# Kernel optimization log

Measured on AMD Instinct MI355X. Metric: run time of the kernel, lower is better.

## Reference

```python
import jax, jax.numpy as jnp
import numpy as np

D = 768  # hidden dim hard-coded in the module


def setup_inputs() -> dict:
    key = jax.random.key(0)
    k1, k2, k3, k4, k5 = jax.random.split(key, 5)
    N, M = 512, 512
    return {
        "text_output": jax.random.normal(k1, (N, D), dtype=jnp.float32),
        "visual_output": jax.random.normal(k2, (M, D), dtype=jnp.float32),
        "W1": jax.random.normal(k3, (D, D), dtype=jnp.float32),
        "W2": jax.random.normal(k4, (D, D), dtype=jnp.float32),
        "W3": jax.random.normal(k5, (D, D), dtype=jnp.float32),
    }


def reference(text_output, visual_output, W1, W2, W3):
    # C[n,m] = tanh( (text @ W1) . visual[m] )
    C = jnp.tanh((text_output @ W1) @ visual_output.T)            # (N, M)
    W2_text = text_output @ W2                                    # (N, D)
    W3_visual = visual_output @ W3.T                              # (M, D)
    # M[n,m,:] = tanh(W2_text[n] + W3_visual[m] * C[n,m])
    Mt = jnp.tanh(W2_text[:, None, :] + W3_visual[None, :, :] * C[..., None])  # (N, M, D)
    # score[n,m] = text[n] . M[n,m]  (replaces the per-row Python loop)
    score = jnp.einsum("nd,nmd->nm", text_output, Mt)             # (N, M)
    return score
```

## Files before the change

### kernel.cpp

```cpp
#include <hip/hip_runtime.h>

#define DD   768
#define NN   512
#define MM   512

#define PRE_K 2.88539008177792681472f

typedef _Float16 h8 __attribute__((ext_vector_type(8)));
typedef __attribute__((ext_vector_type(4))) float f32x4;

__device__ __forceinline__ float fexp(float x) { return __builtin_amdgcn_exp2f(x); }
__device__ __forceinline__ float frcp(float x) { return __builtin_amdgcn_rcpf(x); }
__device__ __forceinline__ float fast_tanh(float x) {
  return 1.0f - 2.0f * frcp(fexp(PRE_K * x) + 1.0f);
}

__device__ __forceinline__ void splitf(float x, ushort& h, ushort& l) {
  const _Float16 hh = (_Float16)x;
  const _Float16 ll = (_Float16)(x - (float)hh);
  h = __builtin_bit_cast(unsigned short, hh);
  l = __builtin_bit_cast(unsigned short, ll);
}

__global__ __launch_bounds__(256) void prep_kernel(
    const float* __restrict__ text, const float* __restrict__ visual,
    const float* __restrict__ W1, const float* __restrict__ W2,
    const float* __restrict__ W3,
    ushort* __restrict__ th, ushort* __restrict__ tl,
    ushort* __restrict__ vh, ushort* __restrict__ vl,
    ushort* __restrict__ w3h, ushort* __restrict__ w3l,
    ushort* __restrict__ w1th, ushort* __restrict__ w1tl,
    ushort* __restrict__ w2th, ushort* __restrict__ w2tl,
    float* __restrict__ out)
{
  __shared__ float Lt[32][33];
  const int b = blockIdx.x;
  const int t = threadIdx.x;

  if (b < 1344) {
    const float* src; ushort *dh, *dl; size_t off;
    if (b < 384)      { src = text;   dh = th;  dl = tl;  off = (size_t)b * 1024; }
    else if (b < 768) { src = visual; dh = vh;  dl = vl;  off = (size_t)(b - 384) * 1024; }
    else              { src = W3;     dh = w3h; dl = w3l; off = (size_t)(b - 768) * 1024; }
    const size_t i = off + (size_t)t * 4;
    const float4 v = *(const float4*)&src[i];
    ushort4 h, l;
    splitf(v.x, h.x, l.x); splitf(v.y, h.y, l.y);
    splitf(v.z, h.z, l.z); splitf(v.w, h.w, l.w);
    *(ushort4*)&dh[i] = h;
    *(ushort4*)&dl[i] = l;
  } else if (b < 2496) {
    const int tt = b - 1344;
    const bool second = tt >= 576;
    const int tile = second ? tt - 576 : tt;
    const float* W = second ? W2 : W1;
    ushort* oh = second ? w2th : w1th;
    ushort* ol = second ? w2tl : w1tl;
    const int k0 = (tile / 24) * 32, j0 = (tile % 24) * 32;
    {
      const int k = t >> 3, j4 = (t & 7) * 4;
      const float4 v = *(const float4*)&W[(size_t)(k0 + k) * DD + j0 + j4];
      Lt[j4 + 0][k] = v.x; Lt[j4 + 1][k] = v.y;
      Lt[j4 + 2][k] = v.z; Lt[j4 + 3][k] = v.w;
    }
    __syncthreads();
    {
      const int j = t >> 3, k4 = (t & 7) * 4;
      ushort4 h, l;
      splitf(Lt[j][k4 + 0], h.x, l.x); splitf(Lt[j][k4 + 1], h.y, l.y);
      splitf(Lt[j][k4 + 2], h.z, l.z); splitf(Lt[j][k4 + 3], h.w, l.w);
      *(ushort4*)&oh[(size_t)(j0 + j) * DD + k0 + k4] = h;
      *(ushort4*)&ol[(size_t)(j0 + j) * DD + k0 + k4] = l;
    }
  } else {
    float* red = (float*)Lt;
    const int u = b - 2496;
    const int n0 = u * 2;
    const int half = t >> 7;
    const int lt = t & 127;

    const float* tr = text + (size_t)(n0 + half) * DD;
    float s = 0.f;
    #pragma unroll
    for (int i = 0; i < DD / 128; ++i) s += tr[lt + i * 128];
    red[t] = s;
    __syncthreads();
    #pragma unroll
    for (int st = 64; st > 0; st >>= 1) {
      if (lt < st) red[t] += red[t + st];
      __syncthreads();
    }
    const float Tn = red[half << 7];
    float4 o; o.x = Tn; o.y = Tn; o.z = Tn; o.w = Tn;
    *(float4*)&out[(size_t)(n0 + half) * MM + lt * 4] = o;
  }
}

#define BK   32
#define LROW 40
#define APL  (32 * LROW)
#define BPL  (64 * LROW)

template <bool ALO>
__device__ __forceinline__ void gemm_core32(
    ushort* __restrict__ As, ushort* __restrict__ Bs,
    const ushort* __restrict__ Ahg, const ushort* __restrict__ Alg,
    const ushort* __restrict__ Bhg, const ushort* __restrict__ Blg,
    int i0, int j0, int nsteps, f32x4* acc)
{
  const int tid = threadIdx.x;
  const int row = tid >> 2;
  const int ks8 = (tid & 3) * 8;
  const bool doA = (row < 32);
  const size_t ga = (size_t)(i0 + row) * DD + ks8;
  const size_t gb = (size_t)(j0 + row) * DD + ks8;
  const int lw = row * LROW + ks8;

  const int lane = tid & 63, wave = tid >> 6;
  const int r15 = lane & 15, quad = lane >> 4;
  const int wr = wave >> 1, wc = wave & 1;
  const int fa = (wr * 16 + r15) * LROW + quad * 8;
  const int fb = (wc * 32 + r15) * LROW + quad * 8;

  h8 pah, pal, pbh, pbl;
  if (doA) {
    pah = *(const h8*)(Ahg + ga);
    if (ALO) pal = *(const h8*)(Alg + ga);
  }
  pbh = *(const h8*)(Bhg + gb);
  pbl = *(const h8*)(Blg + gb);

  int p = 0;
  if (doA) {
    *(h8*)&As[lw] = pah;
    if (ALO) *(h8*)&As[APL + lw] = pal;
  }
  *(h8*)&Bs[lw] = pbh;
  *(h8*)&Bs[BPL + lw] = pbl;
  __syncthreads();

  for (int s = 0; s < nsteps; ++s) {
    const bool more = (s + 1 < nsteps);
    if (more) {
      if (doA) {
        pah = *(const h8*)(Ahg + ga + (s + 1) * BK);
        if (ALO) pal = *(const h8*)(Alg + ga + (s + 1) * BK);
      }
      pbh = *(const h8*)(Bhg + gb + (s + 1) * BK);
      pbl = *(const h8*)(Blg + gb + (s + 1) * BK);
    }
    ushort* Ac = As + p * 2 * APL;
    ushort* Bc = Bs + p * 2 * BPL;
    const h8 a_h = *(const h8*)&Ac[fa];
    h8 a_l; if (ALO) a_l = *(const h8*)&Ac[APL + fa];
    h8 b_h[2], b_l[2];
    #pragma unroll
    for (int c = 0; c < 2; ++c) {
      b_h[c] = *(const h8*)&Bc[fb + c * 16 * LROW];
      b_l[c] = *(const h8*)&Bc[BPL + fb + c * 16 * LROW];
    }
    #pragma unroll
    for (int c = 0; c < 2; ++c)
      acc[c] = __builtin_amdgcn_mfma_f32_16x16x32_f16(a_h, b_h[c], acc[c], 0, 0, 0);
    #pragma unroll
    for (int c = 0; c < 2; ++c)
      acc[c] = __builtin_amdgcn_mfma_f32_16x16x32_f16(a_h, b_l[c], acc[c], 0, 0, 0);
    if (ALO) {
      #pragma unroll
      for (int c = 0; c < 2; ++c)
        acc[c] = __builtin_amdgcn_mfma_f32_16x16x32_f16(a_l, b_h[c], acc[c], 0, 0, 0);
    }
    if (more) {
      const int q = p ^ 1;
      ushort* An = As + q * 2 * APL;
      ushort* Bn = Bs + q * 2 * BPL;
      if (doA) {
        *(h8*)&An[lw] = pah;
        if (ALO) *(h8*)&An[APL + lw] = pal;
      }
      *(h8*)&Bn[lw] = pbh;
      *(h8*)&Bn[BPL + lw] = pbl;
    }
    __syncthreads();
    p ^= 1;
  }
}

__global__ __launch_bounds__(256) void mfma1_kernel(
    const ushort* __restrict__ th, const ushort* __restrict__ tl,
    const ushort* __restrict__ vh, const ushort* __restrict__ vl,
    const ushort* __restrict__ w1th, const ushort* __restrict__ w1tl,
    const ushort* __restrict__ w2th, const ushort* __restrict__ w2tl,
    const ushort* __restrict__ w3h, const ushort* __restrict__ w3l,
    ushort* __restrict__ Ah, ushort* __restrict__ Al,
    float* __restrict__ kw2t, float* __restrict__ kw3v)
{
  __shared__ ushort As[2 * 2 * APL];
  __shared__ ushort Bs[2 * 2 * BPL];

  const int z  = blockIdx.z;
  const int j0 = blockIdx.x * 64;
  const int i0 = blockIdx.y * 32;

  f32x4 acc[2];
  acc[0] = (f32x4){0.f, 0.f, 0.f, 0.f};
  acc[1] = (f32x4){0.f, 0.f, 0.f, 0.f};

  if (z == 0)
    gemm_core32<true >(As, Bs, th, tl, w1th, w1tl, i0, j0, DD / BK, acc);
  else if (z == 1)
    gemm_core32<false>(As, Bs, th, tl, w2th, w2tl, i0, j0, DD / BK, acc);
  else
    gemm_core32<false>(As, Bs, vh, vl, w3h,  w3l,  i0, j0, DD / BK, acc);

  const int lane = threadIdx.x & 63, wave = threadIdx.x >> 6;
  const int r15 = lane & 15, quad = lane >> 4;
  const int wr = wave >> 1, wc = wave & 1;
  if (z == 0) {
    #pragma unroll
    for (int c = 0; c < 2; ++c)
      #pragma unroll
      for (int r = 0; r < 4; ++r) {
        const size_t o = (size_t)(i0 + wr * 16 + quad * 4 + r) * DD
                       + j0 + wc * 32 + c * 16 + r15;
        splitf(acc[c][r], Ah[o], Al[o]);
      }
  } else {
    float* Out = (z == 1) ? kw2t : kw3v;
    #pragma unroll
    for (int c = 0; c < 2; ++c)
      #pragma unroll
      for (int r = 0; r < 4; ++r)
        Out[(size_t)(i0 + wr * 16 + quad * 4 + r) * DD + j0 + wc * 32 + c * 16 + r15] =
            acc[c][r] * PRE_K;
  }
}

#define DCH    64
#define DRANGE 256
#define MLDW   68

__global__ __launch_bounds__(256) void main_kernel(
    const float* __restrict__ text, const float* __restrict__ kw2t,
    const float* __restrict__ kw3v,
    const ushort* __restrict__ Ah, const ushort* __restrict__ Al,
    const ushort* __restrict__ vh, const ushort* __restrict__ vl,
    float* __restrict__ out)
{
  __shared__ float sbuf[2][32 * MLDW];

  const int tid = threadIdx.x;
  const int nl = tid >> 4;
  const int ml = tid & 15;
  const int n0 = blockIdx.y * 16;
  const int m0 = blockIdx.x * 32;
  const int z  = blockIdx.z;
  const int lane = tid & 63, wave = tid >> 6;
  const int r15 = lane & 15, quad = lane >> 4;

  const size_t aoff  = (size_t)(n0 + r15) * DD + wave * (DD / 4) + quad * 8;
  const size_t b0off = (size_t)(m0 + r15) * DD + wave * (DD / 4) + quad * 8;
  const size_t b1off = (size_t)(m0 + 16 + r15) * DD + wave * (DD / 4) + quad * 8;
  const ushort* Ap  = Ah + aoff;
  const ushort* Alp = Al + aoff;
  const ushort* B0h = vh + b0off;
  const ushort* B0l = vl + b0off;
  const ushort* B1h = vh + b1off;
  const ushort* B1l = vl + b1off;

  f32x4 q0 = {0.f, 0.f, 0.f, 0.f}, q1 = {0.f, 0.f, 0.f, 0.f};
  h8 cah  = *(const h8*)Ap;
  h8 cal  = *(const h8*)Alp;
  h8 cb0h = *(const h8*)B0h;
  h8 cb0l = *(const h8*)B0l;
  h8 cb1h = *(const h8*)B1h;
  h8 cb1l = *(const h8*)B1l;
  #pragma unroll
  for (int s = 0; s < (DD / 4) / BK; ++s) {
    h8 nah, nal, nb0h, nb0l, nb1h, nb1l;
    const bool more = (s + 1 < (DD / 4) / BK);
    if (more) {
      nah  = *(const h8*)(Ap  + (s + 1) * BK);
      nal  = *(const h8*)(Alp + (s + 1) * BK);
      nb0h = *(const h8*)(B0h + (s + 1) * BK);
      nb0l = *(const h8*)(B0l + (s + 1) * BK);
      nb1h = *(const h8*)(B1h + (s + 1) * BK);
      nb1l = *(const h8*)(B1l + (s + 1) * BK);
    }
    q0 = __builtin_amdgcn_mfma_f32_16x16x32_f16(cah, cb0h, q0, 0, 0, 0);
    q1 = __builtin_amdgcn_mfma_f32_16x16x32_f16(cah, cb1h, q1, 0, 0, 0);
    q0 = __builtin_amdgcn_mfma_f32_16x16x32_f16(cah, cb0l, q0, 0, 0, 0);
    q1 = __builtin_amdgcn_mfma_f32_16x16x32_f16(cah, cb1l, q1, 0, 0, 0);
    q0 = __builtin_amdgcn_mfma_f32_16x16x32_f16(cal, cb0h, q0, 0, 0, 0);
    q1 = __builtin_amdgcn_mfma_f32_16x16x32_f16(cal, cb1h, q1, 0, 0, 0);
    if (more) { cah = nah; cal = nal; cb0h = nb0h; cb0l = nb0l; cb1h = nb1h; cb1l = nb1l; }
  }

  float (*Qs)[16][33] = (float (*)[16][33])(&sbuf[0][0]);
  #pragma unroll
  for (int r = 0; r < 4; ++r) {
    Qs[wave][quad * 4 + r][r15]      = q0[r];
    Qs[wave][quad * 4 + r][16 + r15] = q1[r];
  }
  __syncthreads();
  float sA = Qs[0][nl][ml];
  sA += Qs[1][nl][ml]; sA += Qs[2][nl][ml]; sA += Qs[3][nl][ml];
  float sB = Qs[0][nl][ml + 16];
  sB += Qs[1][nl][ml + 16]; sB += Qs[2][nl][ml + 16]; sB += Qs[3][nl][ml + 16];
  const float cA = fast_tanh(sA);
  const float cB = fast_tanh(sB);
  __syncthreads();

  const int n  = n0 + nl;
  const int mA = m0 + ml, mB = mA + 16;
  const int dbase = z * DRANGE;

  float4 aA = {0.f, 0.f, 0.f, 0.f};
  float4 aB = {0.f, 0.f, 0.f, 0.f};

  const float* gt = &text[(size_t)n * DD + dbase];
  const float* g2 = &kw2t[(size_t)n * DD + dbase];

  const int srow = tid >> 4;
  const int sc4  = (tid & 15) << 2;
  const float* g3a = &kw3v[(size_t)(m0 + srow) * DD + dbase + sc4];
  const float* g3b = &kw3v[(size_t)(m0 + 16 + srow) * DD + dbase + sc4];
  const int w3a = srow * MLDW + sc4;
  const int w3b = (16 + srow) * MLDW + sc4;

  float4 r3a = *(const float4*)g3a;
  float4 r3b = *(const float4*)g3b;
  int p = 0;
  *(float4*)&sbuf[0][w3a] = r3a;
  *(float4*)&sbuf[0][w3b] = r3b;
  __syncthreads();

  #pragma unroll
  for (int c = 0; c < DRANGE / DCH; ++c) {
    const bool more = (c + 1 < DRANGE / DCH);
    if (more) {
      r3a = *(const float4*)(g3a + (c + 1) * DCH);
      r3b = *(const float4*)(g3b + (c + 1) * DCH);
    }
    const float* bp = sbuf[p];
    const float* gtc = gt + c * DCH;
    const float* g2c = g2 + c * DCH;
    #pragma unroll 4
    for (int j = 0; j < DCH; j += 4) {
      const float4 tv  = *(const float4*)&gtc[j];
      const float4 w2v = *(const float4*)&g2c[j];
      const float4 w3A = *(const float4*)&bp[ml * MLDW + j];
      const float4 w3B = *(const float4*)&bp[(16 + ml) * MLDW + j];
      aA.x = fmaf(tv.x, frcp(fexp(fmaf(w3A.x, cA, w2v.x)) + 1.0f), aA.x);
      aA.y = fmaf(tv.y, frcp(fexp(fmaf(w3A.y, cA, w2v.y)) + 1.0f), aA.y);
      aA.z = fmaf(tv.z, frcp(fexp(fmaf(w3A.z, cA, w2v.z)) + 1.0f), aA.z);
      aA.w = fmaf(tv.w, frcp(fexp(fmaf(w3A.w, cA, w2v.w)) + 1.0f), aA.w);
      aB.x = fmaf(tv.x, frcp(fexp(fmaf(w3B.x, cB, w2v.x)) + 1.0f), aB.x);
      aB.y = fmaf(tv.y, frcp(fexp(fmaf(w3B.y, cB, w2v.y)) + 1.0f), aB.y);
      aB.z = fmaf(tv.z, frcp(fexp(fmaf(w3B.z, cB, w2v.z)) + 1.0f), aB.z);
      aB.w = fmaf(tv.w, frcp(fexp(fmaf(w3B.w, cB, w2v.w)) + 1.0f), aB.w);
    }
    if (more) {
      const int q = p ^ 1;
      *(float4*)&sbuf[q][w3a] = r3a;
      *(float4*)&sbuf[q][w3b] = r3b;
    }
    __syncthreads();
    p ^= 1;
  }

  float* op = out + (size_t)n * MM;
  unsafeAtomicAdd(&op[mA], -2.0f * ((aA.x + aA.y) + (aA.z + aA.w)));
  unsafeAtomicAdd(&op[mB], -2.0f * ((aB.x + aB.y) + (aB.z + aB.w)));
}

extern "C" void kernel_launch(void* const* d_in, const int* in_sizes, int n_in,
                              void* d_out, int out_size, void* d_ws, size_t ws_size,
                              hipStream_t stream) {
  const float* text   = (const float*)d_in[0];
  const float* visual = (const float*)d_in[1];
  const float* W1     = (const float*)d_in[2];
  const float* W2     = (const float*)d_in[3];
  const float* W3     = (const float*)d_in[4];
  float* out = (float*)d_out;

  char* base = (char*)d_ws;
  ushort* th   = (ushort*)(base);
  ushort* tl   = (ushort*)(base + 786432);
  ushort* vh   = (ushort*)(base + 1572864);
  ushort* vl   = (ushort*)(base + 2359296);
  ushort* w1th = (ushort*)(base + 3145728);
  ushort* w1tl = (ushort*)(base + 4325376);
  ushort* w2th = (ushort*)(base + 5505024);
  ushort* w2tl = (ushort*)(base + 6684672);
  ushort* w3h  = (ushort*)(base + 7864320);
  ushort* w3l  = (ushort*)(base + 9043968);
  ushort* Ah   = (ushort*)(base + 10223616);
  ushort* Al   = (ushort*)(base + 11010048);
  float*  kw2t = (float*) (base + 11796480);
  float*  kw3v = (float*) (base + 13369344);

  hipLaunchKernelGGL(prep_kernel, dim3(2752), dim3(256), 0, stream,
                     text, visual, W1, W2, W3,
                     th, tl, vh, vl, w3h, w3l, w1th, w1tl, w2th, w2tl, out);
  hipLaunchKernelGGL(mfma1_kernel, dim3(DD / 64, NN / 32, 3), dim3(256), 0, stream,
                     th, tl, vh, vl, w1th, w1tl, w2th, w2tl, w3h, w3l,
                     Ah, Al, kw2t, kw3v);
  hipLaunchKernelGGL(main_kernel, dim3(MM / 32, NN / 16, 3), dim3(256), 0, stream,
                     text, kw2t, kw3v, Ah, Al, vh, vl, out);
}
```

Before: 142.3 us.

## Reassociate C as text·(visual·W1ᵀ) and stage text/W2 rows in LDS

Computes C by first forming V1 = visual @ W1ᵀ, using an untransposed W1 split, so C becomes text dotted with V1, which drops the W1 transpose tiles from prep. The main kernel now stages text and kw2t rows in shared memory together with kw3v instead of reading them directly from global memory. It uses smaller D chunks, splits D four ways instead of three, and adds an occupancy hint of 4 blocks per CU. The extra z-slice means more atomic adds and some recomputation of C per block.

```diff
diff --git a/kernel.cpp b/kernel.cpp
--- a/kernel.cpp
+++ b/kernel.cpp
@@ -29,7 +29,7 @@
     ushort* __restrict__ th, ushort* __restrict__ tl,
     ushort* __restrict__ vh, ushort* __restrict__ vl,
     ushort* __restrict__ w3h, ushort* __restrict__ w3l,
-    ushort* __restrict__ w1th, ushort* __restrict__ w1tl,
+    ushort* __restrict__ w1h, ushort* __restrict__ w1l,
     ushort* __restrict__ w2th, ushort* __restrict__ w2tl,
     float* __restrict__ out)
 {
@@ -37,11 +37,12 @@
   const int b = blockIdx.x;
   const int t = threadIdx.x;
 
-  if (b < 1344) {
+  if (b < 1920) {
     const float* src; ushort *dh, *dl; size_t off;
-    if (b < 384)      { src = text;   dh = th;  dl = tl;  off = (size_t)b * 1024; }
-    else if (b < 768) { src = visual; dh = vh;  dl = vl;  off = (size_t)(b - 384) * 1024; }
-    else              { src = W3;     dh = w3h; dl = w3l; off = (size_t)(b - 768) * 1024; }
+    if (b < 384)       { src = text;   dh = th;  dl = tl;  off = (size_t)b * 1024; }
+    else if (b < 768)  { src = visual; dh = vh;  dl = vl;  off = (size_t)(b - 384) * 1024; }
+    else if (b < 1344) { src = W3;     dh = w3h; dl = w3l; off = (size_t)(b - 768) * 1024; }
+    else               { src = W1;     dh = w1h; dl = w1l; off = (size_t)(b - 1344) * 1024; }
     const size_t i = off + (size_t)t * 4;
     const float4 v = *(const float4*)&src[i];
     ushort4 h, l;
@@ -50,16 +51,11 @@
     *(ushort4*)&dh[i] = h;
     *(ushort4*)&dl[i] = l;
   } else if (b < 2496) {
-    const int tt = b - 1344;
-    const bool second = tt >= 576;
-    const int tile = second ? tt - 576 : tt;
-    const float* W = second ? W2 : W1;
-    ushort* oh = second ? w2th : w1th;
-    ushort* ol = second ? w2tl : w1tl;
+    const int tile = b - 1920;
     const int k0 = (tile / 24) * 32, j0 = (tile % 24) * 32;
     {
       const int k = t >> 3, j4 = (t & 7) * 4;
-      const float4 v = *(const float4*)&W[(size_t)(k0 + k) * DD + j0 + j4];
+      const float4 v = *(const float4*)&W2[(size_t)(k0 + k) * DD + j0 + j4];
       Lt[j4 + 0][k] = v.x; Lt[j4 + 1][k] = v.y;
       Lt[j4 + 2][k] = v.z; Lt[j4 + 3][k] = v.w;
     }
@@ -69,8 +65,8 @@
       ushort4 h, l;
       splitf(Lt[j][k4 + 0], h.x, l.x); splitf(Lt[j][k4 + 1], h.y, l.y);
       splitf(Lt[j][k4 + 2], h.z, l.z); splitf(Lt[j][k4 + 3], h.w, l.w);
-      *(ushort4*)&oh[(size_t)(j0 + j) * DD + k0 + k4] = h;
-      *(ushort4*)&ol[(size_t)(j0 + j) * DD + k0 + k4] = l;
+      *(ushort4*)&w2th[(size_t)(j0 + j) * DD + k0 + k4] = h;
+      *(ushort4*)&w2tl[(size_t)(j0 + j) * DD + k0 + k4] = l;
     }
   } else {
     float* red = (float*)Lt;
@@ -106,14 +102,14 @@
     ushort* __restrict__ As, ushort* __restrict__ Bs,
     const ushort* __restrict__ Ahg, const ushort* __restrict__ Alg,
     const ushort* __restrict__ Bhg, const ushort* __restrict__ Blg,
-    int i0, int j0, int nsteps, f32x4* acc)
+    int i0, int j0, int k0, int nsteps, f32x4* acc)
 {
   const int tid = threadIdx.x;
   const int row = tid >> 2;
   const int ks8 = (tid & 3) * 8;
   const bool doA = (row < 32);
-  const size_t ga = (size_t)(i0 + row) * DD + ks8;
-  const size_t gb = (size_t)(j0 + row) * DD + ks8;
+  const size_t ga = (size_t)(i0 + row) * DD + k0 + ks8;
+  const size_t gb = (size_t)(j0 + row) * DD + k0 + ks8;
   const int lw = row * LROW + ks8;
 
   const int lane = tid & 63, wave = tid >> 6;
@@ -189,10 +185,10 @@
 __global__ __launch_bounds__(256) void mfma1_kernel(
     const ushort* __restrict__ th, const ushort* __restrict__ tl,
     const ushort* __restrict__ vh, const ushort* __restrict__ vl,
-    const ushort* __restrict__ w1th, const ushort* __restrict__ w1tl,
+    const ushort* __restrict__ w1h, const ushort* __restrict__ w1l,
     const ushort* __restrict__ w2th, const ushort* __restrict__ w2tl,
     const ushort* __restrict__ w3h, const ushort* __restrict__ w3l,
-    ushort* __restrict__ Ah, ushort* __restrict__ Al,
+    ushort* __restrict__ V1th, ushort* __restrict__ V1tl,
     float* __restrict__ kw2t, float* __restrict__ kw3v)
 {
   __shared__ ushort As[2 * 2 * APL];
@@ -207,11 +203,11 @@
   acc[1] = (f32x4){0.f, 0.f, 0.f, 0.f};
 
   if (z == 0)
-    gemm_core32<true >(As, Bs, th, tl, w1th, w1tl, i0, j0, DD / BK, acc);
+    gemm_core32<true >(As, Bs, vh, vl, w1h, w1l,  i0, j0, 0, DD / BK, acc);
   else if (z == 1)
-    gemm_core32<false>(As, Bs, th, tl, w2th, w2tl, i0, j0, DD / BK, acc);
+    gemm_core32<false>(As, Bs, th, tl, w2th, w2tl, i0, j0, 0, DD / BK, acc);
   else
-    gemm_core32<false>(As, Bs, vh, vl, w3h,  w3l,  i0, j0, DD / BK, acc);
+    gemm_core32<false>(As, Bs, vh, vl, w3h, w3l,  i0, j0, 0, DD / BK, acc);
 
   const int lane = threadIdx.x & 63, wave = threadIdx.x >> 6;
   const int r15 = lane & 15, quad = lane >> 4;
@@ -223,7 +219,7 @@
       for (int r = 0; r < 4; ++r) {
         const size_t o = (size_t)(i0 + wr * 16 + quad * 4 + r) * DD
                        + j0 + wc * 32 + c * 16 + r15;
-        splitf(acc[c][r], Ah[o], Al[o]);
+        splitf(acc[c][r], V1th[o], V1tl[o]);
       }
   } else {
     float* Out = (z == 1) ? kw2t : kw3v;
@@ -236,18 +232,18 @@
   }
 }
 
-#define DCH    64
-#define DRANGE 256
-#define MLDW   68
-
-__global__ __launch_bounds__(256) void main_kernel(
+#define DCH    32
+#define DRANGE 192
+#define MLDW   36
+
+__global__ __launch_bounds__(256, 4) void main_kernel(
     const float* __restrict__ text, const float* __restrict__ kw2t,
     const float* __restrict__ kw3v,
-    const ushort* __restrict__ Ah, const ushort* __restrict__ Al,
-    const ushort* __restrict__ vh, const ushort* __restrict__ vl,
+    const ushort* __restrict__ th, const ushort* __restrict__ tl,
+    const ushort* __restrict__ V1th, const ushort* __restrict__ V1tl,
     float* __restrict__ out)
 {
-  __shared__ float sbuf[2][32 * MLDW];
+  __shared__ float sbuf[2][64 * MLDW];
 
   const int tid = threadIdx.x;
   const int nl = tid >> 4;
@@ -261,12 +257,12 @@
   const size_t aoff  = (size_t)(n0 + r15) * DD + wave * (DD / 4) + quad * 8;
   const size_t b0off = (size_t)(m0 + r15) * DD + wave * (DD / 4) + quad * 8;
   const size_t b1off = (size_t)(m0 + 16 + r15) * DD + wave * (DD / 4) + quad * 8;
-  const ushort* Ap  = Ah + aoff;
-  const ushort* Alp = Al + aoff;
-  const ushort* B0h = vh + b0off;
-  const ushort* B0l = vl + b0off;
-  const ushort* B1h = vh + b1off;
-  const ushort* B1l = vl + b1off;
+  const ushort* Ap  = th + aoff;
+  const ushort* Alp = tl + aoff;
+  const ushort* B0h = V1th + b0off;
+  const ushort* B0l = V1tl + b0off;
+  const ushort* B1h = V1th + b1off;
+  const ushort* B1l = V1tl + b1off;
 
   f32x4 q0 = {0.f, 0.f, 0.f, 0.f}, q1 = {0.f, 0.f, 0.f, 0.f};
   h8 cah  = *(const h8*)Ap;
@@ -318,39 +314,36 @@
   float4 aA = {0.f, 0.f, 0.f, 0.f};
   float4 aB = {0.f, 0.f, 0.f, 0.f};
 
-  const float* gt = &text[(size_t)n * DD + dbase];
-  const float* g2 = &kw2t[(size_t)n * DD + dbase];
-
-  const int srow = tid >> 4;
-  const int sc4  = (tid & 15) << 2;
-  const float* g3a = &kw3v[(size_t)(m0 + srow) * DD + dbase + sc4];
-  const float* g3b = &kw3v[(size_t)(m0 + 16 + srow) * DD + dbase + sc4];
-  const int w3a = srow * MLDW + sc4;
-  const int w3b = (16 + srow) * MLDW + sc4;
-
-  float4 r3a = *(const float4*)g3a;
-  float4 r3b = *(const float4*)g3b;
+  const int srow = tid >> 3;
+  const int sc   = (tid & 7) << 2;
+  const float* g1 = (srow < 16)
+      ? &text[(size_t)(n0 + srow) * DD + dbase + sc]
+      : &kw2t[(size_t)(n0 + srow - 16) * DD + dbase + sc];
+  const float* g3 = &kw3v[(size_t)(m0 + srow) * DD + dbase + sc];
+  const int w1 = srow * MLDW + sc;
+  const int w3 = (32 + srow) * MLDW + sc;
+
+  float4 r1 = *(const float4*)g1;
+  float4 r3 = *(const float4*)g3;
   int p = 0;
-  *(float4*)&sbuf[0][w3a] = r3a;
-  *(float4*)&sbuf[0][w3b] = r3b;
+  *(float4*)&sbuf[0][w1] = r1;
+  *(float4*)&sbuf[0][w3] = r3;
   __syncthreads();
 
   #pragma unroll
   for (int c = 0; c < DRANGE / DCH; ++c) {
     const bool more = (c + 1 < DRANGE / DCH);
     if (more) {
-      r3a = *(const float4*)(g3a + (c + 1) * DCH);
-      r3b = *(const float4*)(g3b + (c + 1) * DCH);
+      r1 = *(const float4*)(g1 + (c + 1) * DCH);
+      r3 = *(const float4*)(g3 + (c + 1) * DCH);
     }
     const float* bp = sbuf[p];
-    const float* gtc = gt + c * DCH;
-    const float* g2c = g2 + c * DCH;
     #pragma unroll 4
     for (int j = 0; j < DCH; j += 4) {
-      const float4 tv  = *(const float4*)&gtc[j];
-      const float4 w2v = *(const float4*)&g2c[j];
-      const float4 w3A = *(const float4*)&bp[ml * MLDW + j];
-      const float4 w3B = *(const float4*)&bp[(16 + ml) * MLDW + j];
+      const float4 tv  = *(const float4*)&bp[nl * MLDW + j];
+      const float4 w2v = *(const float4*)&bp[(16 + nl) * MLDW + j];
+      const float4 w3A = *(const float4*)&bp[(32 + ml) * MLDW + j];
+      const float4 w3B = *(const float4*)&bp[(48 + ml) * MLDW + j];
       aA.x = fmaf(tv.x, frcp(fexp(fmaf(w3A.x, cA, w2v.x)) + 1.0f), aA.x);
       aA.y = fmaf(tv.y, frcp(fexp(fmaf(w3A.y, cA, w2v.y)) + 1.0f), aA.y);
       aA.z = fmaf(tv.z, frcp(fexp(fmaf(w3A.z, cA, w2v.z)) + 1.0f), aA.z);
@@ -362,8 +355,8 @@
     }
     if (more) {
       const int q = p ^ 1;
-      *(float4*)&sbuf[q][w3a] = r3a;
-      *(float4*)&sbuf[q][w3b] = r3b;
+      *(float4*)&sbuf[q][w1] = r1;
+      *(float4*)&sbuf[q][w3] = r3;
     }
     __syncthreads();
     p ^= 1;
@@ -389,23 +382,23 @@
   ushort* tl   = (ushort*)(base + 786432);
   ushort* vh   = (ushort*)(base + 1572864);
   ushort* vl   = (ushort*)(base + 2359296);
-  ushort* w1th = (ushort*)(base + 3145728);
-  ushort* w1tl = (ushort*)(base + 4325376);
+  ushort* w1h  = (ushort*)(base + 3145728);
+  ushort* w1l  = (ushort*)(base + 4325376);
   ushort* w2th = (ushort*)(base + 5505024);
   ushort* w2tl = (ushort*)(base + 6684672);
   ushort* w3h  = (ushort*)(base + 7864320);
   ushort* w3l  = (ushort*)(base + 9043968);
-  ushort* Ah   = (ushort*)(base + 10223616);
-  ushort* Al   = (ushort*)(base + 11010048);
+  ushort* V1th = (ushort*)(base + 10223616);
+  ushort* V1tl = (ushort*)(base + 11010048);
   float*  kw2t = (float*) (base + 11796480);
   float*  kw3v = (float*) (base + 13369344);
 
   hipLaunchKernelGGL(prep_kernel, dim3(2752), dim3(256), 0, stream,
                      text, visual, W1, W2, W3,
-                     th, tl, vh, vl, w3h, w3l, w1th, w1tl, w2th, w2tl, out);
+                     th, tl, vh, vl, w3h, w3l, w1h, w1l, w2th, w2tl, out);
   hipLaunchKernelGGL(mfma1_kernel, dim3(DD / 64, NN / 32, 3), dim3(256), 0, stream,
-                     th, tl, vh, vl, w1th, w1tl, w2th, w2tl, w3h, w3l,
-                     Ah, Al, kw2t, kw3v);
-  hipLaunchKernelGGL(main_kernel, dim3(MM / 32, NN / 16, 3), dim3(256), 0, stream,
-                     text, kw2t, kw3v, Ah, Al, vh, vl, out);
-}
+                     th, tl, vh, vl, w1h, w1l, w2th, w2tl, w3h, w3l,
+                     V1th, V1tl, kw2t, kw3v);
+  hipLaunchKernelGGL(main_kernel, dim3(MM / 32, NN / 16, 4), dim3(256), 0, stream,
+                     text, kw2t, kw3v, th, tl, V1th, V1tl, out);
+}
```

After: 132.6 us. -6.8%, faster.
